# Optimization experiments

Measured on AMD Instinct MI355X. Metric: run time of the kernel, lower is better.

## Reference

```python
import jax, jax.numpy as jnp
import numpy as np

R_CUT = 2.5
N_BASIS = 8
BOX_SIZE = 10.0


def radial_encode(r, n, r_cut):
    """Gaussian radial basis on squared distance r: (...,) -> (..., n).
    Centers spread over [0, r_cut], width r_cut/n. (Helper source not given;
    this is the standard RBF encode used in such MD graph nets.)"""
    mu = jnp.linspace(0.0, r_cut, n, dtype=r.dtype)        # (n,)
    sigma = r_cut / n
    d = r[..., None] - mu                                   # (..., n)
    return jnp.exp(-0.5 * (d / sigma) ** 2)


def setup_inputs() -> dict:
    key = jax.random.key(0)
    k1, k2 = jax.random.split(key)
    batch, nodes, deg = 8, 20000, 32
    pos = jax.random.uniform(k1, (batch, nodes, 3), dtype=jnp.float32) * BOX_SIZE
    box = jnp.full((3,), BOX_SIZE, dtype=jnp.float32)
    nbr_idx = jax.random.randint(k2, (nodes, deg), 0, nodes, dtype=jnp.int64)
    return {"pos": pos, "box": box, "nbr_idx": nbr_idx}


def reference(pos, box, nbr_idx):
    # pos: (B, N, 3); box: (3,); nbr_idx: (N, deg)
    ang_box = box / (2.0 * jnp.pi)                          # (3,)
    # edges_read: gather neighbor positions -> (B, N, deg, 3)
    nbr_pos = pos[:, nbr_idx]                               # (B, N, deg, 3)
    edges = nbr_pos - pos[:, :, None]                       # relative displacement
    # periodic-box sin wrap
    edges = ang_box * jnp.sin(edges / ang_box)
    r = jnp.sum(edges ** 2, axis=-1)                        # (B, N, deg) squared dist
    x = radial_encode(r, N_BASIS, R_CUT)                    # (B, N, deg, 8)
    xv = x[..., None] * edges[..., None, :]                 # (B, N, deg, 8, 3) outer product
    # edges_reduce: sum over neighbor axis
    y = jnp.sum(x, axis=2)                                  # (B, N, 8)
    yv = jnp.sum(xv, axis=2)                                # (B, N, 8, 3)
    return (y, yv)
```

## Files before the change

### kernel.cpp

```cpp
#include <hip/hip_runtime.h>

static constexpr int BATCH = 8;
static constexpr int NODES = 20000;
static constexpr int DEG   = 32;
static constexpr int NB    = 8;

static constexpr float SIGMA = 2.5f / 8.0f;
static constexpr float ISIG  = 1.0f / SIGMA;

__global__ __launch_bounds__(256)
void graph_embed_kernel(const float* __restrict__ pos,
                        const float* __restrict__ box,
                        const int*   __restrict__ nbr,
                        float* __restrict__ out)
{
    const int t = blockIdx.x * blockDim.x + threadIdx.x;
    if (t >= BATCH * NODES) return;
    const int b = t / NODES;
    const int i = t - b * NODES;

    const float inv2pi = 0.15915494309189535f;
    const float ab0 = box[0] * inv2pi;
    const float ab1 = box[1] * inv2pi;
    const float ab2 = box[2] * inv2pi;
    const float ia0 = 1.0f / ab0;
    const float ia1 = 1.0f / ab1;
    const float ia2 = 1.0f / ab2;

    const float* __restrict__ pb = pos + (size_t)b * NODES * 3;
    const float p0 = pb[3 * i + 0];
    const float p1 = pb[3 * i + 1];
    const float p2 = pb[3 * i + 2];

    float bk[NB];
#pragma unroll
    for (int k = 0; k < NB; ++k) bk[k] = (2.5f * (float)k / 7.0f) * ISIG;

    float y0[NB], v0[NB], v1[NB], v2[NB];
#pragma unroll
    for (int k = 0; k < NB; ++k) { y0[k] = 0.f; v0[k] = 0.f; v1[k] = 0.f; v2[k] = 0.f; }

    const int* __restrict__ row = nbr + (size_t)i * DEG;

#pragma unroll 4
    for (int j = 0; j < DEG; ++j) {
        const int idx = row[j];
        const float* __restrict__ q = pb + (size_t)idx * 3;
        const float d0 = q[0] - p0;
        const float d1 = q[1] - p1;
        const float d2 = q[2] - p2;
        const float e0 = ab0 * __sinf(d0 * ia0);
        const float e1 = ab1 * __sinf(d1 * ia1);
        const float e2 = ab2 * __sinf(d2 * ia2);
        const float r  = fmaf(e0, e0, fmaf(e1, e1, e2 * e2));

#pragma unroll
        for (int k = 0; k < NB; ++k) {
            const float tt = fmaf(r, ISIG, -bk[k]);
            const float x  = __expf(-0.5f * tt * tt);
            y0[k] += x;
            v0[k] = fmaf(x, e0, v0[k]);
            v1[k] = fmaf(x, e1, v1[k]);
            v2[k] = fmaf(x, e2, v2[k]);
        }
    }

    float* __restrict__ yptr = out + (size_t)t * NB;
    *(float4*)(yptr + 0) = make_float4(y0[0], y0[1], y0[2], y0[3]);
    *(float4*)(yptr + 4) = make_float4(y0[4], y0[5], y0[6], y0[7]);

    float* __restrict__ vptr = out + (size_t)BATCH * NODES * NB + (size_t)t * (NB * 3);
    *(float4*)(vptr +  0) = make_float4(v0[0], v1[0], v2[0], v0[1]);
    *(float4*)(vptr +  4) = make_float4(v1[1], v2[1], v0[2], v1[2]);
    *(float4*)(vptr +  8) = make_float4(v2[2], v0[3], v1[3], v2[3]);
    *(float4*)(vptr + 12) = make_float4(v0[4], v1[4], v2[4], v0[5]);
    *(float4*)(vptr + 16) = make_float4(v1[5], v2[5], v0[6], v1[6]);
    *(float4*)(vptr + 20) = make_float4(v2[6], v0[7], v1[7], v2[7]);
}

extern "C" void kernel_launch(void* const* d_in, const int* in_sizes, int n_in,
                              void* d_out, int out_size, void* d_ws, size_t ws_size,
                              hipStream_t stream) {
    const float* pos = (const float*)d_in[0];
    const float* box = (const float*)d_in[1];
    const int*   nbr = (const int*)d_in[2];
    float* out = (float*)d_out;

    const int total = BATCH * NODES;
    const int block = 256;
    const int grid  = (total + block - 1) / block;
    graph_embed_kernel<<<grid, block, 0, stream>>>(pos, box, nbr, out);
}
```

Baseline: 99.72 us.

## Use Gaussian recurrence, pack positions to float4, vectorize and prefetch neighbor gathers

The eight per-edge Gaussian exponentials are replaced by two exp2 calls plus a multiplicative recurrence using precomputed constant ratios, which cuts transcendental work. Positions are first repacked into float4 in workspace by a separate kernel, so each neighbor gather becomes one 16-byte load. Neighbor indices are read as int4 and the next group is prefetched in software. Costs are an extra kernel launch and pass over positions, more registers for the prefetch, and some numerical drift from the recurrence.

```diff
diff --git a/kernel.cpp b/kernel.cpp
--- a/kernel.cpp
+++ b/kernel.cpp
@@ -5,11 +5,24 @@
 static constexpr int DEG   = 32;
 static constexpr int NB    = 8;
 
-static constexpr float SIGMA = 2.5f / 8.0f;
-static constexpr float ISIG  = 1.0f / SIGMA;
+#if defined(__has_builtin) && __has_builtin(__builtin_amdgcn_exp2f)
+#define EXP2F(x) __builtin_amdgcn_exp2f(x)
+#else
+#define EXP2F(x) exp2f(x)
+#endif
+
+static constexpr float C1 = -7.3865986f;
+static constexpr float C2 = 5.2761417f;
 
 __global__ __launch_bounds__(256)
-void graph_embed_kernel(const float* __restrict__ pos,
+void pack_pos_kernel(const float* __restrict__ pos, float4* __restrict__ pos4) {
+    const int t = blockIdx.x * blockDim.x + threadIdx.x;
+    if (t >= BATCH * NODES) return;
+    pos4[t] = make_float4(pos[3 * t + 0], pos[3 * t + 1], pos[3 * t + 2], 0.0f);
+}
+
+__global__ __launch_bounds__(256)
+void graph_embed_kernel(const float4* __restrict__ pos4,
                         const float* __restrict__ box,
                         const int*   __restrict__ nbr,
                         float* __restrict__ out)
@@ -27,48 +40,117 @@
     const float ia1 = 1.0f / ab1;
     const float ia2 = 1.0f / ab2;
 
+    float h[NB - 1];
+#pragma unroll
+    for (int k = 0; k < NB - 1; ++k)
+        h[k] = __expf(-0.6530612245f * (float)(2 * k + 1));
+
+    const float4* __restrict__ pb = pos4 + (size_t)b * NODES;
+    const float4 p = pb[i];
+
+    float y0[NB], v0[NB], v1[NB], v2[NB];
+#pragma unroll
+    for (int k = 0; k < NB; ++k) { y0[k] = 0.f; v0[k] = 0.f; v1[k] = 0.f; v2[k] = 0.f; }
+
+    const int4* __restrict__ row = (const int4*)(nbr + (size_t)i * DEG);
+
+    int4 idx = row[0];
+    float4 q0 = pb[idx.x], q1 = pb[idx.y], q2 = pb[idx.z], q3 = pb[idx.w];
+
+#pragma unroll
+    for (int grp = 0; grp < DEG / 4; ++grp) {
+        float4 n0, n1, n2, n3;
+        if (grp + 1 < DEG / 4) {
+            const int4 nidx = row[grp + 1];
+            n0 = pb[nidx.x]; n1 = pb[nidx.y]; n2 = pb[nidx.z]; n3 = pb[nidx.w];
+        }
+        const float4 qs[4] = { q0, q1, q2, q3 };
+#pragma unroll
+        for (int jj = 0; jj < 4; ++jj) {
+            const float4 q = qs[jj];
+            const float e0 = ab0 * __sinf((q.x - p.x) * ia0);
+            const float e1 = ab1 * __sinf((q.y - p.y) * ia1);
+            const float e2 = ab2 * __sinf((q.z - p.z) * ia2);
+            const float r  = fmaf(e0, e0, fmaf(e1, e1, e2 * e2));
+
+            const float g = EXP2F(r * C2);
+            float x = EXP2F(r * r * C1);
+#pragma unroll
+            for (int k = 0; k < NB; ++k) {
+                y0[k] += x;
+                v0[k] = fmaf(x, e0, v0[k]);
+                v1[k] = fmaf(x, e1, v1[k]);
+                v2[k] = fmaf(x, e2, v2[k]);
+                if (k < NB - 1) x = x * g * h[k];
+            }
+        }
+        q0 = n0; q1 = n1; q2 = n2; q3 = n3;
+    }
+
+    float* __restrict__ yptr = out + (size_t)t * NB;
+    *(float4*)(yptr + 0) = make_float4(y0[0], y0[1], y0[2], y0[3]);
+    *(float4*)(yptr + 4) = make_float4(y0[4], y0[5], y0[6], y0[7]);
+
+    float* __restrict__ vptr = out + (size_t)BATCH * NODES * NB + (size_t)t * (NB * 3);
+    *(float4*)(vptr +  0) = make_float4(v0[0], v1[0], v2[0], v0[1]);
+    *(float4*)(vptr +  4) = make_float4(v1[1], v2[1], v0[2], v1[2]);
+    *(float4*)(vptr +  8) = make_float4(v2[2], v0[3], v1[3], v2[3]);
+    *(float4*)(vptr + 12) = make_float4(v0[4], v1[4], v2[4], v0[5]);
+    *(float4*)(vptr + 16) = make_float4(v1[5], v2[5], v0[6], v1[6]);
+    *(float4*)(vptr + 20) = make_float4(v2[6], v0[7], v1[7], v2[7]);
+}
+
+__global__ __launch_bounds__(256)
+void graph_embed_fallback_kernel(const float* __restrict__ pos,
+                                 const float* __restrict__ box,
+                                 const int*   __restrict__ nbr,
+                                 float* __restrict__ out)
+{
+    const int t = blockIdx.x * blockDim.x + threadIdx.x;
+    if (t >= BATCH * NODES) return;
+    const int b = t / NODES;
+    const int i = t - b * NODES;
+
+    const float inv2pi = 0.15915494309189535f;
+    const float ab0 = box[0] * inv2pi, ab1 = box[1] * inv2pi, ab2 = box[2] * inv2pi;
+    const float ia0 = 1.0f / ab0, ia1 = 1.0f / ab1, ia2 = 1.0f / ab2;
+
+    float h[NB - 1];
+#pragma unroll
+    for (int k = 0; k < NB - 1; ++k)
+        h[k] = __expf(-0.6530612245f * (float)(2 * k + 1));
+
     const float* __restrict__ pb = pos + (size_t)b * NODES * 3;
-    const float p0 = pb[3 * i + 0];
-    const float p1 = pb[3 * i + 1];
-    const float p2 = pb[3 * i + 2];
-
-    float bk[NB];
-#pragma unroll
-    for (int k = 0; k < NB; ++k) bk[k] = (2.5f * (float)k / 7.0f) * ISIG;
+    const float p0 = pb[3 * i + 0], p1 = pb[3 * i + 1], p2 = pb[3 * i + 2];
 
     float y0[NB], v0[NB], v1[NB], v2[NB];
 #pragma unroll
     for (int k = 0; k < NB; ++k) { y0[k] = 0.f; v0[k] = 0.f; v1[k] = 0.f; v2[k] = 0.f; }
 
     const int* __restrict__ row = nbr + (size_t)i * DEG;
-
 #pragma unroll 4
     for (int j = 0; j < DEG; ++j) {
         const int idx = row[j];
         const float* __restrict__ q = pb + (size_t)idx * 3;
-        const float d0 = q[0] - p0;
-        const float d1 = q[1] - p1;
-        const float d2 = q[2] - p2;
-        const float e0 = ab0 * __sinf(d0 * ia0);
-        const float e1 = ab1 * __sinf(d1 * ia1);
-        const float e2 = ab2 * __sinf(d2 * ia2);
+        const float e0 = ab0 * __sinf((q[0] - p0) * ia0);
+        const float e1 = ab1 * __sinf((q[1] - p1) * ia1);
+        const float e2 = ab2 * __sinf((q[2] - p2) * ia2);
         const float r  = fmaf(e0, e0, fmaf(e1, e1, e2 * e2));
-
+        const float g = EXP2F(r * C2);
+        float x = EXP2F(r * r * C1);
 #pragma unroll
         for (int k = 0; k < NB; ++k) {
-            const float tt = fmaf(r, ISIG, -bk[k]);
-            const float x  = __expf(-0.5f * tt * tt);
             y0[k] += x;
             v0[k] = fmaf(x, e0, v0[k]);
             v1[k] = fmaf(x, e1, v1[k]);
             v2[k] = fmaf(x, e2, v2[k]);
+            if (k < NB - 1) x = x * g * h[k];
         }
     }
 
     float* __restrict__ yptr = out + (size_t)t * NB;
     *(float4*)(yptr + 0) = make_float4(y0[0], y0[1], y0[2], y0[3]);
     *(float4*)(yptr + 4) = make_float4(y0[4], y0[5], y0[6], y0[7]);
-
     float* __restrict__ vptr = out + (size_t)BATCH * NODES * NB + (size_t)t * (NB * 3);
     *(float4*)(vptr +  0) = make_float4(v0[0], v1[0], v2[0], v0[1]);
     *(float4*)(vptr +  4) = make_float4(v1[1], v2[1], v0[2], v1[2]);
@@ -89,5 +171,13 @@
     const int total = BATCH * NODES;
     const int block = 256;
     const int grid  = (total + block - 1) / block;
-    graph_embed_kernel<<<grid, block, 0, stream>>>(pos, box, nbr, out);
+
+    const size_t packed_bytes = (size_t)total * sizeof(float4);
+    if (ws_size >= packed_bytes) {
+        float4* pos4 = (float4*)d_ws;
+        pack_pos_kernel<<<grid, block, 0, stream>>>(pos, pos4);
+        graph_embed_kernel<<<grid, block, 0, stream>>>(pos4, box, nbr, out);
+    } else {
+        graph_embed_fallback_kernel<<<grid, block, 0, stream>>>(pos, box, nbr, out);
+    }
 }
```

Result: no change. 100.5 us (+0.7%).
